# Kernel optimization log

Measured on AMD Instinct MI355X. Metric: run time of the kernel, lower is better.

Reference implementation:

```python
import jax, jax.numpy as jnp
from jax import lax
import numpy as np

S, LC = 4096, 16
WORD_V, CHAR_V, TAG_V = 100000, 128, 64
WE, WH, CE, CH = 256, 256, 64, 128


def _p(key, shape, scale=0.1):
    return (scale * jax.random.normal(key, shape)).astype(jnp.float32)


def setup_inputs() -> dict:
    key = jax.random.key(0)
    ks = jax.random.split(key, 16)
    return {
        "sent": jax.random.randint(ks[0], (S,), 0, WORD_V),
        "chars": jax.random.randint(ks[1], (S, LC), 0, CHAR_V),
        "char_lens": jax.random.randint(ks[2], (S,), 1, LC + 1),
        "char_emb": _p(ks[3], (CHAR_V, CE)),
        "word_emb": _p(ks[4], (WORD_V, WE)),
        "cW_ih": _p(ks[5], (4 * CH, CE)),
        "cW_hh": _p(ks[6], (4 * CH, CH)),
        "cb_ih": _p(ks[7], (4 * CH,)),
        "cb_hh": _p(ks[8], (4 * CH,)),
        "wW_ih": _p(ks[9], (4 * WH, WE + CH)),
        "wW_hh": _p(ks[10], (4 * WH, WH)),
        "wb_ih": _p(ks[11], (4 * WH,)),
        "wb_hh": _p(ks[12], (4 * WH,)),
        "tagW": _p(ks[13], (TAG_V, WH)),
        "tagb": _p(ks[14], (TAG_V,)),
    }


def lstm_scan(xs, W_ih, W_hh, b_ih, b_hh):
    """xs: [T, B, D] -> all hidden states [T, B, H] (torch gate order i,f,g,o)."""
    H = W_hh.shape[1]
    B = xs.shape[1]
    bias = b_ih + b_hh

    def step(carry, x):
        h, c = carry
        g = x @ W_ih.T + h @ W_hh.T + bias  # [B, 4H]
        i, f, gg, o = jnp.split(g, 4, axis=-1)
        c = jax.nn.sigmoid(f) * c + jax.nn.sigmoid(i) * jnp.tanh(gg)
        h = jax.nn.sigmoid(o) * jnp.tanh(c)
        return (h, c), h

    init = (jnp.zeros((B, H), xs.dtype), jnp.zeros((B, H), xs.dtype))
    _, hs = lax.scan(step, init, xs)
    return hs


def reference(sent, chars, char_lens, char_emb, word_emb,
              cW_ih, cW_hh, cb_ih, cb_hh,
              wW_ih, wW_hh, wb_ih, wb_hh, tagW, tagb):
    embeds = word_emb[sent]                              # [S, WE]
    # Char LSTM: all words batched; [LC, S, CE]
    char_x = char_emb[chars].transpose(1, 0, 2)
    char_hs = lstm_scan(char_x, cW_ih, cW_hh, cb_ih, cb_hh)  # [LC, S, CH]
    # final hidden state at each word's true length (batch-1 per-word LSTM equiv.)
    char_final = char_hs[char_lens - 1, jnp.arange(S)]   # [S, CH]
    combined = jnp.concatenate([embeds, char_final], axis=1)  # [S, WE+CH]
    lstm_out = lstm_scan(combined[:, None, :], wW_ih, wW_hh, wb_ih, wb_hh)[:, 0]  # [S, WH]
    tag_space = lstm_out @ tagW.T + tagb                 # [S, TAG_V]
    return jax.nn.log_softmax(tag_space, axis=1)
```

## Files before the change

kernel.cpp:

```cpp
#include <hip/hip_runtime.h>

#define S_LEN 4096
#define LCH   16
#define CED   64
#define CHD   128
#define WED   256
#define WHD   256
#define TAGV  64

typedef _Float16 hf;
typedef _Float16 hf2 __attribute__((ext_vector_type(2)));

__device__ __forceinline__ float dot2f(hf2 a, hf2 b, float acc) {
#if __has_builtin(__builtin_amdgcn_fdot2)
  return __builtin_amdgcn_fdot2(a, b, acc, false);
#else
  return acc + (float)a.x * (float)b.x + (float)a.y * (float)b.y;
#endif
}

__device__ __forceinline__ int dot4i8(int a, int b, int c) {
#if __has_builtin(__builtin_amdgcn_sdot4)
  return __builtin_amdgcn_sdot4(a, b, c, false);
#else
  int r = c;
  r += (int)(signed char)(a)       * (int)(signed char)(b);
  r += (int)(signed char)(a >> 8)  * (int)(signed char)(b >> 8);
  r += (int)(signed char)(a >> 16) * (int)(signed char)(b >> 16);
  r += (int)(signed char)(a >> 24) * (int)(signed char)(b >> 24);
  return r;
#endif
}

__device__ __forceinline__ float ex2(float x) {
#if __has_builtin(__builtin_amdgcn_exp2f)
  return __builtin_amdgcn_exp2f(x);
#else
  return __exp2f(x);
#endif
}
__device__ __forceinline__ float rcp_(float x) {
#if __has_builtin(__builtin_amdgcn_rcpf)
  return __builtin_amdgcn_rcpf(x);
#else
  return 1.f / x;
#endif
}

template <int C> __device__ __forceinline__ int dppi(int x) {
  return __builtin_amdgcn_mov_dpp(x, C, 0xf, 0xf, false);
}
template <int C> __device__ __forceinline__ float dppf(float x) {
  return __int_as_float(__builtin_amdgcn_mov_dpp(__float_as_int(x), C, 0xf, 0xf, false));
}

__device__ __forceinline__ float sigf(float x) { return 1.f / (1.f + __expf(-x)); }
__device__ __forceinline__ float tanhf_(float x) {
  float a = fabsf(x);
  float e = __expf(-2.f * a);
  float t = (1.f - e) / (1.f + e);
  return copysignf(t, x);
}

__global__ __launch_bounds__(256) void k_char_lstm(
    const int* __restrict__ chars, const int* __restrict__ char_lens,
    const float* __restrict__ char_emb,
    const float* __restrict__ cW_ih, const float* __restrict__ cW_hh,
    const float* __restrict__ cb_ih, const float* __restrict__ cb_hh,
    float* __restrict__ char_final) {
  __shared__ hf emb_s[128 * CED];
  __shared__ hf h_s[2][8][CHD];
  __shared__ int chars_s[8 * LCH];
  __shared__ int lens_s[8];

  const int tid = threadIdx.x;
  const int u = tid >> 1, kh = tid & 1;
  const int w0 = blockIdx.x * 8;

  for (int i = tid; i < 128 * CED; i += 256) emb_s[i] = (hf)char_emb[i];
  for (int i = tid; i < 8 * LCH; i += 256) chars_s[i] = chars[w0 * LCH + i];
  if (tid < 8) lens_s[tid] = char_lens[w0 + tid];
  {
    hf* hz = &h_s[0][0][0];
    for (int i = tid; i < 8 * CHD; i += 256) hz[i] = (hf)0.f;
  }

  hf2 wih[4][16];
  hf2 whh[4][32];
  float bq[4];
#pragma unroll
  for (int q = 0; q < 4; ++q) {
    const int r = q * CHD + u;
    const float* pi = cW_ih + r * CED + 32 * kh;
#pragma unroll
    for (int j = 0; j < 16; ++j) { hf2 v; v.x = (hf)pi[2*j]; v.y = (hf)pi[2*j+1]; wih[q][j] = v; }
    const float* ph = cW_hh + r * CHD + 64 * kh;
#pragma unroll
    for (int j = 0; j < 32; ++j) { hf2 v; v.x = (hf)ph[2*j]; v.y = (hf)ph[2*j+1]; whh[q][j] = v; }
    bq[q] = cb_ih[r] + cb_hh[r];
  }
  float c[8];
#pragma unroll
  for (int w = 0; w < 8; ++w) c[w] = 0.f;
  __syncthreads();

  for (int t = 0; t < LCH; ++t) {
    const int cur = t & 1, nxt = cur ^ 1;
#pragma unroll
    for (int w = 0; w < 8; ++w) {
      const int cidx = chars_s[w * LCH + t];
      const hf2* xr = (const hf2*)(emb_s + cidx * CED + 32 * kh);
      const hf2* hr = (const hf2*)(&h_s[cur][w][64 * kh]);
      float a0 = 0.f, a1 = 0.f, a2 = 0.f, a3 = 0.f;
#pragma unroll
      for (int j = 0; j < 16; ++j) {
        hf2 xv = xr[j];
        a0 = dot2f(wih[0][j], xv, a0); a1 = dot2f(wih[1][j], xv, a1);
        a2 = dot2f(wih[2][j], xv, a2); a3 = dot2f(wih[3][j], xv, a3);
      }
#pragma unroll
      for (int j = 0; j < 32; ++j) {
        hf2 hv = hr[j];
        a0 = dot2f(whh[0][j], hv, a0); a1 = dot2f(whh[1][j], hv, a1);
        a2 = dot2f(whh[2][j], hv, a2); a3 = dot2f(whh[3][j], hv, a3);
      }
      a0 += __shfl_xor(a0, 1); a1 += __shfl_xor(a1, 1);
      a2 += __shfl_xor(a2, 1); a3 += __shfl_xor(a3, 1);
      const float ig = sigf(a0 + bq[0]);
      const float fg = sigf(a1 + bq[1]);
      const float gg = tanhf_(a2 + bq[2]);
      const float og = sigf(a3 + bq[3]);
      c[w] = fg * c[w] + ig * gg;
      const float hn = og * tanhf_(c[w]);
      if (kh == 0) {
        h_s[nxt][w][u] = (hf)hn;
        if (t == lens_s[w] - 1) char_final[(w0 + w) * CHD + u] = hn;
      }
    }
    __syncthreads();
  }
}

__global__ __launch_bounds__(1024) void k_wxp(
    const int* __restrict__ sent, const float* __restrict__ word_emb,
    const float* __restrict__ char_final,
    const float* __restrict__ wW_ih, const float* __restrict__ wb_ih,
    const float* __restrict__ wb_hh, float* __restrict__ xp) {
  __shared__ float comb[16][WED + CHD];
  const int tid = threadIdx.x;
  const int s0 = blockIdx.x * 16;
  for (int i = tid; i < 16 * WED; i += 1024) {
    const int w = i / WED, k = i % WED;
    comb[w][k] = word_emb[(long)sent[s0 + w] * WED + k];
  }
  for (int i = tid; i < 16 * CHD; i += 1024) {
    const int w = i / CHD, k = i % CHD;
    comb[w][WED + k] = char_final[(s0 + w) * CHD + k];
  }
  __syncthreads();

  const int e = tid >> 9, r = tid & 511;
  const int gate = 256 * (r & 3) + 2 * (r >> 2) + e;
  const float bias = wb_ih[gate] + wb_hh[gate];
  float acc[16];
#pragma unroll
  for (int w = 0; w < 16; ++w) acc[w] = bias;
  const float* wrow = wW_ih + gate * (WED + CHD);
  for (int kc = 0; kc < WED + CHD; kc += 64) {
    float wv[64];
#pragma unroll
    for (int i = 0; i < 64; ++i) wv[i] = wrow[kc + i];
#pragma unroll
    for (int w = 0; w < 16; ++w) {
      const float4* cr = (const float4*)&comb[w][kc];
      float a = 0.f;
#pragma unroll
      for (int i = 0; i < 16; ++i) {
        float4 cv = cr[i];
        a += wv[4*i] * cv.x + wv[4*i+1] * cv.y + wv[4*i+2] * cv.z + wv[4*i+3] * cv.w;
      }
      acc[w] += a;
    }
  }
#pragma unroll
  for (int w = 0; w < 16; ++w) xp[(long)(s0 + w) * 1024 + tid] = acc[w];
}

__global__ __launch_bounds__(512, 2) void k_word_lstm(
    const float* __restrict__ wW_hh, const float* __restrict__ xp,
    float* __restrict__ h_all) {
  __shared__ int hq[2][WHD / 4];
  const int t = threadIdx.x;
  const int p = t >> 2, l = t & 3;
  const int uA = 2 * p, uB = 2 * p + 1;

  int wqA0[16], wqA1[16], wqA2[16], wqA3[16];
  int wqB0[16], wqB1[16], wqB2[16], wqB3[16];
  float mA0, mA1, mA2, mA3, mB0, mB1, mB2, mB3;

#define ROWMAX(mdst, row) do {                                                  \
    const float4* wr_ = (const float4*)(wW_hh + (long)(row) * WHD + 64 * l);    \
    float m_ = 0.f;                                                             \
    _Pragma("unroll")                                                           \
    for (int j = 0; j < 16; ++j) {                                              \
      float4 v = wr_[j];                                                        \
      m_ = fmaxf(m_, fmaxf(fmaxf(fabsf(v.x), fabsf(v.y)),                       \
                           fmaxf(fabsf(v.z), fabsf(v.w))));                     \
    }                                                                           \
    m_ = fmaxf(m_, dppf<0xB1>(m_)); m_ = fmaxf(m_, dppf<0x4E>(m_));             \
    (mdst) = m_;                                                                \
  } while (0)

  ROWMAX(mA0, 0 * WHD + uA); ROWMAX(mA1, 1 * WHD + uA);
  ROWMAX(mA2, 2 * WHD + uA); ROWMAX(mA3, 3 * WHD + uA);
  ROWMAX(mB0, 0 * WHD + uB); ROWMAX(mB1, 1 * WHD + uB);
  ROWMAX(mB2, 2 * WHD + uB); ROWMAX(mB3, 3 * WHD + uB);
#undef ROWMAX

#define QROW(dst, row, mreg) do {                                               \
    const float4* wr_ = (const float4*)(wW_hh + (long)(row) * WHD + 64 * l);    \
    const float r_ = ((mreg) > 0.f) ? 127.f / (mreg) : 0.f;                     \
    _Pragma("unroll")                                                           \
    for (int j = 0; j < 16; ++j) {                                              \
      float4 v = wr_[j];                                                        \
      const int b0 = (int)rintf(v.x * r_) & 255;                                \
      const int b1 = (int)rintf(v.y * r_) & 255;                                \
      const int b2 = (int)rintf(v.z * r_) & 255;                                \
      const int b3 = (int)rintf(v.w * r_) & 255;                                \
      dst[j] = b0 | (b1 << 8) | (b2 << 16) | (b3 << 24);                        \
    }                                                                           \
  } while (0)

  QROW(wqA0, 0 * WHD + uA, mA0); QROW(wqA1, 1 * WHD + uA, mA1);
  QROW(wqA2, 2 * WHD + uA, mA2); QROW(wqA3, 3 * WHD + uA, mA3);
  QROW(wqB0, 0 * WHD + uB, mB0); QROW(wqB1, 1 * WHD + uB, mB1);
  QROW(wqB2, 2 * WHD + uB, mB2); QROW(wqB3, 3 * WHD + uB, mB3);
#undef QROW

  const float mselA = (l & 1) ? ((l & 2) ? mA3 : mA1) : ((l & 2) ? mA2 : mA0);
  const float mselB = (l & 1) ? ((l & 2) ? mB3 : mB1) : ((l & 2) ? mB2 : mB0);
  const float dqA = mselA * (1.f / (127.f * 127.f));
  const float dqB = mselB * (1.f / (127.f * 127.f));
  const float em = (l == 2) ? -2.885390082f : -1.442695041f;
  const float s_ = (l == 2) ? 2.f : 1.f;
  const float d_ = (l == 2) ? -1.f : 0.f;

  if (t < 32) { int4 z; z.x = z.y = z.z = z.w = 0; ((int4*)hq)[t] = z; }
  float cA = 0.f, cB = 0.f;
  __syncthreads();

  const float* xbase = xp + t;
  float* hout = h_all + 2 * p;

#define DOT4W(j, W) do {                                                        \
    aA0 = dot4i8(wqA0[j], (W), aA0); aA1 = dot4i8(wqA1[j], (W), aA1);           \
    aA2 = dot4i8(wqA2[j], (W), aA2); aA3 = dot4i8(wqA3[j], (W), aA3);           \
    aB0 = dot4i8(wqB0[j], (W), aB0); aB1 = dot4i8(wqB1[j], (W), aB1);           \
    aB2 = dot4i8(wqB2[j], (W), aB2); aB3 = dot4i8(wqB3[j], (W), aB3);           \
  } while (0)

#define STEP(T, XA, XB, CUR) do {                                               \
    const int4* hp_ = (const int4*)(&hq[CUR][0]) + l * 4;                       \
    int4 h0 = hp_[0], h1 = hp_[1], h2 = hp_[2], h3 = hp_[3];                    \
    int aA0 = 0, aA1 = 0, aA2 = 0, aA3 = 0;                                     \
    int aB0 = 0, aB1 = 0, aB2 = 0, aB3 = 0;                                     \
    DOT4W(0, h0.x);  DOT4W(1, h0.y);  DOT4W(2, h0.z);  DOT4W(3, h0.w);          \
    DOT4W(4, h1.x);  DOT4W(5, h1.y);  DOT4W(6, h1.z);  DOT4W(7, h1.w);          \
    DOT4W(8, h2.x);  DOT4W(9, h2.y);  DOT4W(10, h2.z); DOT4W(11, h2.w);         \
    DOT4W(12, h3.x); DOT4W(13, h3.y); DOT4W(14, h3.z); DOT4W(15, h3.w);         \
                        \
    int rA0 = (l & 1) ? aA1 : aA0, gA0 = (l & 1) ? aA0 : aA1;                   \
    int rA1 = (l & 1) ? aA3 : aA2, gA1 = (l & 1) ? aA2 : aA3;                   \
    rA0 += dppi<0xB1>(gA0); rA1 += dppi<0xB1>(gA1);                             \
    int oAi = (l & 2) ? rA1 : rA0, gA2 = (l & 2) ? rA0 : rA1;                   \
    oAi += dppi<0x4E>(gA2);                                                     \
    int rB0 = (l & 1) ? aB1 : aB0, gB0 = (l & 1) ? aB0 : aB1;                   \
    int rB1 = (l & 1) ? aB3 : aB2, gB1 = (l & 1) ? aB2 : aB3;                   \
    rB0 += dppi<0xB1>(gB0); rB1 += dppi<0xB1>(gB1);                             \
    int oBi = (l & 2) ? rB1 : rB0, gB2 = (l & 2) ? rB0 : rB1;                   \
    oBi += dppi<0x4E>(gB2);                                                     \
    const float gfA = fmaf((float)oAi, dqA, (XA));                              \
    const float gfB = fmaf((float)oBi, dqB, (XB));                              \
    const float actA = fmaf(s_, rcp_(1.f + ex2(em * gfA)), d_);                 \
    const float actB = fmaf(s_, rcp_(1.f + ex2(em * gfB)), d_);                 \
    const float iA = dppf<0x00>(actA), fA = dppf<0x55>(actA);                   \
    const float gA = dppf<0xAA>(actA), oA = dppf<0xFF>(actA);                   \
    const float iB = dppf<0x00>(actB), fB = dppf<0x55>(actB);                   \
    const float gB = dppf<0xAA>(actB), oB = dppf<0xFF>(actB);                   \
    cA = fmaf(fA, cA, iA * gA);                                                 \
    cB = fmaf(fB, cB, iB * gB);                                                 \
    const float tcA = fmaf(2.f, rcp_(1.f + ex2(-2.885390082f * cA)), -1.f);     \
    const float tcB = fmaf(2.f, rcp_(1.f + ex2(-2.885390082f * cB)), -1.f);     \
    const float hnA = oA * tcA, hnB = oB * tcB;                                 \
    if (l == 0) {                                                               \
      const int qa = (int)rintf(hnA * 127.f) & 255;                             \
      const int qb = (int)rintf(hnB * 127.f) & 255;                             \
      ((unsigned short*)&hq[(CUR) ^ 1][0])[p] = (unsigned short)(qa | (qb << 8));\
    }                                                                           \
    if (l == 1) {                                                               \
      float2 h2v; h2v.x = hnA; h2v.y = hnB;                                     \
      *(float2*)(hout + (long)(T) * WHD) = h2v;                                 \
    }                                                                           \
    asm volatile("s_waitcnt lgkmcnt(0)\n\ts_barrier" ::: "memory");             \
  } while (0)

  float A0a = xbase[0],    A0b = xbase[512];
  float A1a = xbase[1024], A1b = xbase[1536];
  float A2a = xbase[2048], A2b = xbase[2560];
  float A3a = xbase[3072], A3b = xbase[3584];
  for (int t0 = 0; t0 < S_LEN; t0 += 8) {
    const float* pb = xbase + (long)(t0 + 4) * 1024;
    const float B0a = pb[0],    B0b = pb[512];
    const float B1a = pb[1024], B1b = pb[1536];
    const float B2a = pb[2048], B2b = pb[2560];
    const float B3a = pb[3072], B3b = pb[3584];
    STEP(t0 + 0, A0a, A0b, 0); STEP(t0 + 1, A1a, A1b, 1);
    STEP(t0 + 2, A2a, A2b, 0); STEP(t0 + 3, A3a, A3b, 1);
    if (t0 + 8 < S_LEN) {
      const float* pa = xbase + (long)(t0 + 8) * 1024;
      A0a = pa[0];    A0b = pa[512];
      A1a = pa[1024]; A1b = pa[1536];
      A2a = pa[2048]; A2b = pa[2560];
      A3a = pa[3072]; A3b = pa[3584];
    }
    STEP(t0 + 4, B0a, B0b, 0); STEP(t0 + 5, B1a, B1b, 1);
    STEP(t0 + 6, B2a, B2b, 0); STEP(t0 + 7, B3a, B3b, 1);
  }
#undef STEP
#undef DOT4W
}

__global__ __launch_bounds__(64) void k_tag(
    const float* __restrict__ h_all, const float* __restrict__ tagW,
    const float* __restrict__ tagb, float* __restrict__ out) {
  __shared__ float hrow[WHD];
  const int s = blockIdx.x, t = threadIdx.x;
  for (int i = t; i < WHD; i += 64) hrow[i] = h_all[(long)s * WHD + i];
  __syncthreads();
  const float4* wr = (const float4*)(tagW + t * WHD);
  const float4* hr = (const float4*)hrow;
  float a = tagb[t];
#pragma unroll
  for (int i = 0; i < 64; ++i) {
    float4 w4 = wr[i], h4 = hr[i];
    a += w4.x * h4.x + w4.y * h4.y + w4.z * h4.z + w4.w * h4.w;
  }
  float m = a;
#pragma unroll
  for (int d = 1; d < 64; d <<= 1) m = fmaxf(m, __shfl_xor(m, d));
  const float e = __expf(a - m);
  float sum = e;
#pragma unroll
  for (int d = 1; d < 64; d <<= 1) sum += __shfl_xor(sum, d);
  out[(long)s * TAGV + t] = (a - m) - logf(sum);
}

extern "C" void kernel_launch(void* const* d_in, const int* in_sizes, int n_in,
                              void* d_out, int out_size, void* d_ws, size_t ws_size,
                              hipStream_t stream) {
  const int* sent       = (const int*)d_in[0];
  const int* chars      = (const int*)d_in[1];
  const int* char_lens  = (const int*)d_in[2];
  const float* char_emb = (const float*)d_in[3];
  const float* word_emb = (const float*)d_in[4];
  const float* cW_ih    = (const float*)d_in[5];
  const float* cW_hh    = (const float*)d_in[6];
  const float* cb_ih    = (const float*)d_in[7];
  const float* cb_hh    = (const float*)d_in[8];
  const float* wW_ih    = (const float*)d_in[9];
  const float* wW_hh    = (const float*)d_in[10];
  const float* wb_ih    = (const float*)d_in[11];
  const float* wb_hh    = (const float*)d_in[12];
  const float* tagW     = (const float*)d_in[13];
  const float* tagb     = (const float*)d_in[14];
  float* out = (float*)d_out;

  char* ws = (char*)d_ws;
  float* char_final = (float*)ws;
  float* xp         = (float*)(ws + ((size_t)2 << 20));
  float* h_all      = (float*)(ws + ((size_t)20 << 20));

  hipLaunchKernelGGL(k_char_lstm, dim3(512), dim3(256), 0, stream,
                     chars, char_lens, char_emb, cW_ih, cW_hh, cb_ih, cb_hh, char_final);
  hipLaunchKernelGGL(k_wxp, dim3(256), dim3(1024), 0, stream,
                     sent, word_emb, char_final, wW_ih, wb_ih, wb_hh, xp);
  hipLaunchKernelGGL(k_word_lstm, dim3(1), dim3(512), 0, stream, wW_hh, xp, h_all);
  hipLaunchKernelGGL(k_tag, dim3(4096), dim3(64), 0, stream, h_all, tagW, tagb, out);
}
```

Baseline: 4.129 ms.

## Spread word LSTM over 1024 threads, one unit per quad; speed char LSTM math

The sequential word-LSTM kernel now runs 1024 threads, each quad of lanes owning a single hidden unit instead of two. This halves the per-thread int8 dot work on the serial critical path but doubles the number of waves that meet at each per-step barrier. The xp gate layout in k_wxp is remapped to match. The char LSTM now loads h and x as vectors, replaces the shuffle with DPP, and uses exp2/rcp activations. k_wxp also loads its weights as float4.

```diff
diff --git a/kernel.cpp b/kernel.cpp
--- a/kernel.cpp
+++ b/kernel.cpp
@@ -11,11 +11,14 @@
 typedef _Float16 hf;
 typedef _Float16 hf2 __attribute__((ext_vector_type(2)));
 
-__device__ __forceinline__ float dot2f(hf2 a, hf2 b, float acc) {
+union PK2 { int i; hf2 h; };
+
+__device__ __forceinline__ float dot2i(int a, int b, float acc) {
+  PK2 ua, ub; ua.i = a; ub.i = b;
 #if __has_builtin(__builtin_amdgcn_fdot2)
-  return __builtin_amdgcn_fdot2(a, b, acc, false);
+  return __builtin_amdgcn_fdot2(ua.h, ub.h, acc, false);
 #else
-  return acc + (float)a.x * (float)b.x + (float)a.y * (float)b.y;
+  return acc + (float)ua.h.x * (float)ub.h.x + (float)ua.h.y * (float)ub.h.y;
 #endif
 }
 
@@ -54,12 +57,11 @@
   return __int_as_float(__builtin_amdgcn_mov_dpp(__float_as_int(x), C, 0xf, 0xf, false));
 }
 
-__device__ __forceinline__ float sigf(float x) { return 1.f / (1.f + __expf(-x)); }
-__device__ __forceinline__ float tanhf_(float x) {
-  float a = fabsf(x);
-  float e = __expf(-2.f * a);
-  float t = (1.f - e) / (1.f + e);
-  return copysignf(t, x);
+__device__ __forceinline__ float fsig(float x) {
+  return rcp_(1.f + ex2(-1.442695041f * x));
+}
+__device__ __forceinline__ float ftanh(float x) {
+  return fmaf(2.f, rcp_(1.f + ex2(-2.885390082f * x)), -1.f);
 }
 
 __global__ __launch_bounds__(256) void k_char_lstm(
@@ -85,18 +87,18 @@
     for (int i = tid; i < 8 * CHD; i += 256) hz[i] = (hf)0.f;
   }
 
-  hf2 wih[4][16];
-  hf2 whh[4][32];
+  int wih[4][16];
+  int whh[4][32];
   float bq[4];
 #pragma unroll
   for (int q = 0; q < 4; ++q) {
     const int r = q * CHD + u;
     const float* pi = cW_ih + r * CED + 32 * kh;
 #pragma unroll
-    for (int j = 0; j < 16; ++j) { hf2 v; v.x = (hf)pi[2*j]; v.y = (hf)pi[2*j+1]; wih[q][j] = v; }
+    for (int j = 0; j < 16; ++j) { PK2 v; v.h.x = (hf)pi[2*j]; v.h.y = (hf)pi[2*j+1]; wih[q][j] = v.i; }
     const float* ph = cW_hh + r * CHD + 64 * kh;
 #pragma unroll
-    for (int j = 0; j < 32; ++j) { hf2 v; v.x = (hf)ph[2*j]; v.y = (hf)ph[2*j+1]; whh[q][j] = v; }
+    for (int j = 0; j < 32; ++j) { PK2 v; v.h.x = (hf)ph[2*j]; v.h.y = (hf)ph[2*j+1]; whh[q][j] = v.i; }
     bq[q] = cb_ih[r] + cb_hh[r];
   }
   float c[8];
@@ -109,29 +111,32 @@
 #pragma unroll
     for (int w = 0; w < 8; ++w) {
       const int cidx = chars_s[w * LCH + t];
-      const hf2* xr = (const hf2*)(emb_s + cidx * CED + 32 * kh);
-      const hf2* hr = (const hf2*)(&h_s[cur][w][64 * kh]);
+      const int4* xr4 = (const int4*)(emb_s + cidx * CED + 32 * kh);
+      const int4* hr4 = (const int4*)(&h_s[cur][w][64 * kh]);
+      int xi[16], hi[32];
+#pragma unroll
+      for (int j = 0; j < 4; ++j) *(int4*)(xi + 4 * j) = xr4[j];
+#pragma unroll
+      for (int j = 0; j < 8; ++j) *(int4*)(hi + 4 * j) = hr4[j];
       float a0 = 0.f, a1 = 0.f, a2 = 0.f, a3 = 0.f;
 #pragma unroll
       for (int j = 0; j < 16; ++j) {
-        hf2 xv = xr[j];
-        a0 = dot2f(wih[0][j], xv, a0); a1 = dot2f(wih[1][j], xv, a1);
-        a2 = dot2f(wih[2][j], xv, a2); a3 = dot2f(wih[3][j], xv, a3);
+        a0 = dot2i(wih[0][j], xi[j], a0); a1 = dot2i(wih[1][j], xi[j], a1);
+        a2 = dot2i(wih[2][j], xi[j], a2); a3 = dot2i(wih[3][j], xi[j], a3);
       }
 #pragma unroll
       for (int j = 0; j < 32; ++j) {
-        hf2 hv = hr[j];
-        a0 = dot2f(whh[0][j], hv, a0); a1 = dot2f(whh[1][j], hv, a1);
-        a2 = dot2f(whh[2][j], hv, a2); a3 = dot2f(whh[3][j], hv, a3);
+        a0 = dot2i(whh[0][j], hi[j], a0); a1 = dot2i(whh[1][j], hi[j], a1);
+        a2 = dot2i(whh[2][j], hi[j], a2); a3 = dot2i(whh[3][j], hi[j], a3);
       }
-      a0 += __shfl_xor(a0, 1); a1 += __shfl_xor(a1, 1);
-      a2 += __shfl_xor(a2, 1); a3 += __shfl_xor(a3, 1);
-      const float ig = sigf(a0 + bq[0]);
-      const float fg = sigf(a1 + bq[1]);
-      const float gg = tanhf_(a2 + bq[2]);
-      const float og = sigf(a3 + bq[3]);
-      c[w] = fg * c[w] + ig * gg;
-      const float hn = og * tanhf_(c[w]);
+      a0 += dppf<0xB1>(a0); a1 += dppf<0xB1>(a1);
+      a2 += dppf<0xB1>(a2); a3 += dppf<0xB1>(a3);
+      const float ig = fsig(a0 + bq[0]);
+      const float fg = fsig(a1 + bq[1]);
+      const float gg = ftanh(a2 + bq[2]);
+      const float og = fsig(a3 + bq[3]);
+      c[w] = fmaf(fg, c[w], ig * gg);
+      const float hn = og * ftanh(c[w]);
       if (kh == 0) {
         h_s[nxt][w][u] = (hf)hn;
         if (t == lens_s[w] - 1) char_final[(w0 + w) * CHD + u] = hn;
@@ -159,17 +164,17 @@
   }
   __syncthreads();
 
-  const int e = tid >> 9, r = tid & 511;
-  const int gate = 256 * (r & 3) + 2 * (r >> 2) + e;
+  const int gate = 256 * (tid & 3) + (tid >> 2);
   const float bias = wb_ih[gate] + wb_hh[gate];
   float acc[16];
 #pragma unroll
   for (int w = 0; w < 16; ++w) acc[w] = bias;
   const float* wrow = wW_ih + gate * (WED + CHD);
   for (int kc = 0; kc < WED + CHD; kc += 64) {
-    float wv[64];
-#pragma unroll
-    for (int i = 0; i < 64; ++i) wv[i] = wrow[kc + i];
+    const float4* wr4 = (const float4*)(wrow + kc);
+    float4 wv[16];
+#pragma unroll
+    for (int i = 0; i < 16; ++i) wv[i] = wr4[i];
 #pragma unroll
     for (int w = 0; w < 16; ++w) {
       const float4* cr = (const float4*)&comb[w][kc];
@@ -177,7 +182,7 @@
 #pragma unroll
       for (int i = 0; i < 16; ++i) {
         float4 cv = cr[i];
-        a += wv[4*i] * cv.x + wv[4*i+1] * cv.y + wv[4*i+2] * cv.z + wv[4*i+3] * cv.w;
+        a += wv[i].x * cv.x + wv[i].y * cv.y + wv[i].z * cv.z + wv[i].w * cv.w;
       }
       acc[w] += a;
     }
@@ -186,17 +191,15 @@
   for (int w = 0; w < 16; ++w) xp[(long)(s0 + w) * 1024 + tid] = acc[w];
 }
 
-__global__ __launch_bounds__(512, 2) void k_word_lstm(
+__global__ __launch_bounds__(1024, 4) void k_word_lstm(
     const float* __restrict__ wW_hh, const float* __restrict__ xp,
     float* __restrict__ h_all) {
   __shared__ int hq[2][WHD / 4];
   const int t = threadIdx.x;
   const int p = t >> 2, l = t & 3;
-  const int uA = 2 * p, uB = 2 * p + 1;
-
-  int wqA0[16], wqA1[16], wqA2[16], wqA3[16];
-  int wqB0[16], wqB1[16], wqB2[16], wqB3[16];
-  float mA0, mA1, mA2, mA3, mB0, mB1, mB2, mB3;
+
+  float m0, m1, m2, m3;
+  int wq0[16], wq1[16], wq2[16], wq3[16];
 
 #define ROWMAX(mdst, row) do {                                                  \
     const float4* wr_ = (const float4*)(wW_hh + (long)(row) * WHD + 64 * l);    \
@@ -211,10 +214,8 @@
     (mdst) = m_;                                                                \
   } while (0)
 
-  ROWMAX(mA0, 0 * WHD + uA); ROWMAX(mA1, 1 * WHD + uA);
-  ROWMAX(mA2, 2 * WHD + uA); ROWMAX(mA3, 3 * WHD + uA);
-  ROWMAX(mB0, 0 * WHD + uB); ROWMAX(mB1, 1 * WHD + uB);
-  ROWMAX(mB2, 2 * WHD + uB); ROWMAX(mB3, 3 * WHD + uB);
+  ROWMAX(m0, 0 * WHD + p); ROWMAX(m1, 1 * WHD + p);
+  ROWMAX(m2, 2 * WHD + p); ROWMAX(m3, 3 * WHD + p);
 #undef ROWMAX
 
 #define QROW(dst, row, mreg) do {                                               \
@@ -231,103 +232,71 @@
     }                                                                           \
   } while (0)
 
-  QROW(wqA0, 0 * WHD + uA, mA0); QROW(wqA1, 1 * WHD + uA, mA1);
-  QROW(wqA2, 2 * WHD + uA, mA2); QROW(wqA3, 3 * WHD + uA, mA3);
-  QROW(wqB0, 0 * WHD + uB, mB0); QROW(wqB1, 1 * WHD + uB, mB1);
-  QROW(wqB2, 2 * WHD + uB, mB2); QROW(wqB3, 3 * WHD + uB, mB3);
+  QROW(wq0, 0 * WHD + p, m0); QROW(wq1, 1 * WHD + p, m1);
+  QROW(wq2, 2 * WHD + p, m2); QROW(wq3, 3 * WHD + p, m3);
 #undef QROW
 
-  const float mselA = (l & 1) ? ((l & 2) ? mA3 : mA1) : ((l & 2) ? mA2 : mA0);
-  const float mselB = (l & 1) ? ((l & 2) ? mB3 : mB1) : ((l & 2) ? mB2 : mB0);
-  const float dqA = mselA * (1.f / (127.f * 127.f));
-  const float dqB = mselB * (1.f / (127.f * 127.f));
+  const float ma = (l & 1) ? m1 : m0;
+  const float mb = (l & 1) ? m3 : m2;
+  const float msel = (l & 2) ? mb : ma;
+  const float dq = msel * (1.f / (127.f * 127.f));
   const float em = (l == 2) ? -2.885390082f : -1.442695041f;
   const float s_ = (l == 2) ? 2.f : 1.f;
   const float d_ = (l == 2) ? -1.f : 0.f;
 
-  if (t < 32) { int4 z; z.x = z.y = z.z = z.w = 0; ((int4*)hq)[t] = z; }
-  float cA = 0.f, cB = 0.f;
+  if (t < 128) ((int*)hq)[t] = 0;
+  float c = 0.f;
   __syncthreads();
 
   const float* xbase = xp + t;
-  float* hout = h_all + 2 * p;
-
-#define DOT4W(j, W) do {                                                        \
-    aA0 = dot4i8(wqA0[j], (W), aA0); aA1 = dot4i8(wqA1[j], (W), aA1);           \
-    aA2 = dot4i8(wqA2[j], (W), aA2); aA3 = dot4i8(wqA3[j], (W), aA3);           \
-    aB0 = dot4i8(wqB0[j], (W), aB0); aB1 = dot4i8(wqB1[j], (W), aB1);           \
-    aB2 = dot4i8(wqB2[j], (W), aB2); aB3 = dot4i8(wqB3[j], (W), aB3);           \
+  float* hout = h_all + p;
+
+#define D4(j, W) do {                                                           \
+    a0 = dot4i8(wq0[j], (W), a0); a1 = dot4i8(wq1[j], (W), a1);                 \
+    a2 = dot4i8(wq2[j], (W), a2); a3 = dot4i8(wq3[j], (W), a3);                 \
   } while (0)
 
-#define STEP(T, XA, XB, CUR) do {                                               \
-    const int4* hp_ = (const int4*)(&hq[CUR][0]) + l * 4;                       \
+#define STEP(T, XV, CUR) do {                                                   \
+    const int4* hp_ = (const int4*)(&hq[CUR][0]) + 4 * l;                       \
     int4 h0 = hp_[0], h1 = hp_[1], h2 = hp_[2], h3 = hp_[3];                    \
-    int aA0 = 0, aA1 = 0, aA2 = 0, aA3 = 0;                                     \
-    int aB0 = 0, aB1 = 0, aB2 = 0, aB3 = 0;                                     \
-    DOT4W(0, h0.x);  DOT4W(1, h0.y);  DOT4W(2, h0.z);  DOT4W(3, h0.w);          \
-    DOT4W(4, h1.x);  DOT4W(5, h1.y);  DOT4W(6, h1.z);  DOT4W(7, h1.w);          \
-    DOT4W(8, h2.x);  DOT4W(9, h2.y);  DOT4W(10, h2.z); DOT4W(11, h2.w);         \
-    DOT4W(12, h3.x); DOT4W(13, h3.y); DOT4W(14, h3.z); DOT4W(15, h3.w);         \
-                        \
-    int rA0 = (l & 1) ? aA1 : aA0, gA0 = (l & 1) ? aA0 : aA1;                   \
-    int rA1 = (l & 1) ? aA3 : aA2, gA1 = (l & 1) ? aA2 : aA3;                   \
-    rA0 += dppi<0xB1>(gA0); rA1 += dppi<0xB1>(gA1);                             \
-    int oAi = (l & 2) ? rA1 : rA0, gA2 = (l & 2) ? rA0 : rA1;                   \
-    oAi += dppi<0x4E>(gA2);                                                     \
-    int rB0 = (l & 1) ? aB1 : aB0, gB0 = (l & 1) ? aB0 : aB1;                   \
-    int rB1 = (l & 1) ? aB3 : aB2, gB1 = (l & 1) ? aB2 : aB3;                   \
-    rB0 += dppi<0xB1>(gB0); rB1 += dppi<0xB1>(gB1);                             \
-    int oBi = (l & 2) ? rB1 : rB0, gB2 = (l & 2) ? rB0 : rB1;                   \
-    oBi += dppi<0x4E>(gB2);                                                     \
-    const float gfA = fmaf((float)oAi, dqA, (XA));                              \
-    const float gfB = fmaf((float)oBi, dqB, (XB));                              \
-    const float actA = fmaf(s_, rcp_(1.f + ex2(em * gfA)), d_);                 \
-    const float actB = fmaf(s_, rcp_(1.f + ex2(em * gfB)), d_);                 \
-    const float iA = dppf<0x00>(actA), fA = dppf<0x55>(actA);                   \
-    const float gA = dppf<0xAA>(actA), oA = dppf<0xFF>(actA);                   \
-    const float iB = dppf<0x00>(actB), fB = dppf<0x55>(actB);                   \
-    const float gB = dppf<0xAA>(actB), oB = dppf<0xFF>(actB);                   \
-    cA = fmaf(fA, cA, iA * gA);                                                 \
-    cB = fmaf(fB, cB, iB * gB);                                                 \
-    const float tcA = fmaf(2.f, rcp_(1.f + ex2(-2.885390082f * cA)), -1.f);     \
-    const float tcB = fmaf(2.f, rcp_(1.f + ex2(-2.885390082f * cB)), -1.f);     \
-    const float hnA = oA * tcA, hnB = oB * tcB;                                 \
-    if (l == 0) {                                                               \
-      const int qa = (int)rintf(hnA * 127.f) & 255;                             \
-      const int qb = (int)rintf(hnB * 127.f) & 255;                             \
-      ((unsigned short*)&hq[(CUR) ^ 1][0])[p] = (unsigned short)(qa | (qb << 8));\
-    }                                                                           \
-    if (l == 1) {                                                               \
-      float2 h2v; h2v.x = hnA; h2v.y = hnB;                                     \
-      *(float2*)(hout + (long)(T) * WHD) = h2v;                                 \
-    }                                                                           \
+    int a0 = 0, a1 = 0, a2 = 0, a3 = 0;                                         \
+    D4(0, h0.x);  D4(1, h0.y);  D4(2, h0.z);  D4(3, h0.w);                      \
+    D4(4, h1.x);  D4(5, h1.y);  D4(6, h1.z);  D4(7, h1.w);                      \
+    D4(8, h2.x);  D4(9, h2.y);  D4(10, h2.z); D4(11, h2.w);                     \
+    D4(12, h3.x); D4(13, h3.y); D4(14, h3.z); D4(15, h3.w);                     \
+    int r0 = (l & 1) ? a1 : a0, g0 = (l & 1) ? a0 : a1;                         \
+    int r1 = (l & 1) ? a3 : a2, g1 = (l & 1) ? a2 : a3;                         \
+    r0 += dppi<0xB1>(g0); r1 += dppi<0xB1>(g1);                                 \
+    int oi = (l & 2) ? r1 : r0, g2 = (l & 2) ? r0 : r1;                         \
+    oi += dppi<0x4E>(g2);                                                       \
+    const float gf = fmaf((float)oi, dq, (XV));                                 \
+    const float act = fmaf(s_, rcp_(1.f + ex2(em * gf)), d_);                   \
+    const float i_ = dppf<0x00>(act), f_ = dppf<0x55>(act);                     \
+    const float g_ = dppf<0xAA>(act), o_ = dppf<0xFF>(act);                     \
+    c = fmaf(f_, c, i_ * g_);                                                   \
+    const float tc = fmaf(2.f, rcp_(1.f + ex2(-2.885390082f * c)), -1.f);       \
+    const float hn = o_ * tc;                                                   \
+    if (l == 0) ((signed char*)&hq[(CUR) ^ 1][0])[p] =                          \
+        (signed char)(int)rintf(hn * 127.f);                                    \
+    if (l == 1) hout[(long)(T) * WHD] = hn;                                     \
     asm volatile("s_waitcnt lgkmcnt(0)\n\ts_barrier" ::: "memory");             \
   } while (0)
 
-  float A0a = xbase[0],    A0b = xbase[512];
-  float A1a = xbase[1024], A1b = xbase[1536];
-  float A2a = xbase[2048], A2b = xbase[2560];
-  float A3a = xbase[3072], A3b = xbase[3584];
+  float xA0 = xbase[0], xA1 = xbase[1024], xA2 = xbase[2048], xA3 = xbase[3072];
   for (int t0 = 0; t0 < S_LEN; t0 += 8) {
     const float* pb = xbase + (long)(t0 + 4) * 1024;
-    const float B0a = pb[0],    B0b = pb[512];
-    const float B1a = pb[1024], B1b = pb[1536];
-    const float B2a = pb[2048], B2b = pb[2560];
-    const float B3a = pb[3072], B3b = pb[3584];
-    STEP(t0 + 0, A0a, A0b, 0); STEP(t0 + 1, A1a, A1b, 1);
-    STEP(t0 + 2, A2a, A2b, 0); STEP(t0 + 3, A3a, A3b, 1);
+    const float xB0 = pb[0], xB1 = pb[1024], xB2 = pb[2048], xB3 = pb[3072];
+    STEP(t0 + 0, xA0, 0); STEP(t0 + 1, xA1, 1);
+    STEP(t0 + 2, xA2, 0); STEP(t0 + 3, xA3, 1);
     if (t0 + 8 < S_LEN) {
       const float* pa = xbase + (long)(t0 + 8) * 1024;
-      A0a = pa[0];    A0b = pa[512];
-      A1a = pa[1024]; A1b = pa[1536];
-      A2a = pa[2048]; A2b = pa[2560];
-      A3a = pa[3072]; A3b = pa[3584];
+      xA0 = pa[0]; xA1 = pa[1024]; xA2 = pa[2048]; xA3 = pa[3072];
     }
-    STEP(t0 + 4, B0a, B0b, 0); STEP(t0 + 5, B1a, B1b, 1);
-    STEP(t0 + 6, B2a, B2b, 0); STEP(t0 + 7, B3a, B3b, 1);
+    STEP(t0 + 4, xB0, 0); STEP(t0 + 5, xB1, 1);
+    STEP(t0 + 6, xB2, 0); STEP(t0 + 7, xB3, 1);
   }
 #undef STEP
-#undef DOT4W
+#undef D4
 }
 
 __global__ __launch_bounds__(64) void k_tag(
@@ -384,6 +353,6 @@
                      chars, char_lens, char_emb, cW_ih, cW_hh, cb_ih, cb_hh, char_final);
   hipLaunchKernelGGL(k_wxp, dim3(256), dim3(1024), 0, stream,
                      sent, word_emb, char_final, wW_ih, wb_ih, wb_hh, xp);
-  hipLaunchKernelGGL(k_word_lstm, dim3(1), dim3(512), 0, stream, wW_hh, xp, h_all);
+  hipLaunchKernelGGL(k_word_lstm, dim3(1), dim3(1024), 0, stream, wW_hh, xp, h_all);
   hipLaunchKernelGGL(k_tag, dim3(4096), dim3(64), 0, stream, h_all, tagW, tagb, out);
 }
```

Result: no change. 4.104 ms (-0.6%).
